# Optimization experiments

Hardware: AMD Instinct MI355X
Metric: run time of the kernel (lower is better)

## Reference

```python
import jax, jax.numpy as jnp
import numpy as np

IN_FEATURES = 4096
OUT_FEATURES = 4096
NNZ = 838860
BATCH = 512


def setup_inputs() -> dict:
    key = jax.random.key(0)
    kx, kr, kc, kv, kb = jax.random.split(key, 5)
    x = jax.random.normal(kx, (BATCH, IN_FEATURES), dtype=jnp.float32)
    row_idx = jax.random.randint(kr, (NNZ,), 0, OUT_FEATURES, dtype=jnp.int64)
    col_idx = jax.random.randint(kc, (NNZ,), 0, IN_FEATURES, dtype=jnp.int64)
    values = jax.random.normal(kv, (NNZ,), dtype=jnp.float32)
    bias = jax.random.normal(kb, (OUT_FEATURES,), dtype=jnp.float32)
    return {"x": x, "row_idx": row_idx, "col_idx": col_idx,
            "values": values, "bias": bias}


def reference(x, row_idx, col_idx, values, bias):
    # COO sparse linear: y[b, row] += x[b, col] * val, then add bias.
    x_flat = x.reshape(-1, IN_FEATURES)                    # [B, in]
    weighted = x_flat[:, col_idx] * values                 # [B, nnz]
    out = jnp.zeros((x_flat.shape[0], OUT_FEATURES), dtype=x.dtype)
    out = out.at[:, row_idx].add(weighted)                 # scatter-add per row
    out = out + bias
    return out.reshape(x.shape[:-1] + (OUT_FEATURES,))
```

## Files before the change

kernel.cpp:

```cpp
#include <hip/hip_runtime.h>

#define IN_F    4096
#define OUT_F   4096
#define K_DIM   4096
#define NNZ_C   838860
#define BATCH   512
#define BK      32
#define BM      128
#define BN      128

typedef short bf16x8 __attribute__((ext_vector_type(8)));
typedef float f32x4  __attribute__((ext_vector_type(4)));

__device__ __forceinline__ unsigned short f2bf(float f) {
    unsigned u = __float_as_uint(f);
    u += 0x7fffu + ((u >> 16) & 1u);
    return (unsigned short)(u >> 16);
}
__device__ __forceinline__ void gload_lds16(const void* g, void* l) {
    __builtin_amdgcn_global_load_lds(
        (const __attribute__((address_space(1))) unsigned int*)g,
        (__attribute__((address_space(3))) unsigned int*)l, 16, 0, 0);
}

#define N_WZ   (OUT_F * K_DIM / 8)
__global__ void zero_w(uint4* __restrict__ Wz) {
    int i = blockIdx.x * 256 + threadIdx.x;
    Wz[i] = make_uint4(0, 0, 0, 0);
}
#define ZW_BLOCKS (N_WZ / 256)

#define N_CVT   (BATCH * K_DIM / 8)
#define N_OUT   (BATCH * OUT_F / 4)
#define NS_BLK  ((NNZ_C / 4 + 255) / 256)
#define NC_BLK  (N_CVT / 256)
#define NB_BLK  (N_OUT / 256)
__global__ void scatcvt(const int* __restrict__ row_idx,
                        const int* __restrict__ col_idx,
                        const float* __restrict__ values,
                        unsigned short* __restrict__ W,
                        const float* __restrict__ x,
                        unsigned short* __restrict__ xb,
                        const float* __restrict__ bias,
                        float* __restrict__ out) {
    int b = blockIdx.x;
    if (b < NS_BLK) {
        int i = b * 256 + threadIdx.x;
        if (i >= NNZ_C / 4) return;
        int4   r4 = ((const int4*)row_idx)[i];
        int4   c4 = ((const int4*)col_idx)[i];
        float4 v4 = ((const float4*)values)[i];
#pragma unroll
        for (int j = 0; j < 4; ++j) {
            int r = (&r4.x)[j], c = (&c4.x)[j];
            float v = (&v4.x)[j];
            unsigned idx = (unsigned)r * K_DIM + (unsigned)c;
            unsigned short h = f2bf(v);
            unsigned data = (idx & 1u) ? ((unsigned)h << 16) : (unsigned)h;
            unsigned long long addr = (unsigned long long)(W + (idx & ~1u));
            asm volatile("global_atomic_pk_add_bf16 %0, %1, off"
                         :: "v"(addr), "v"(data) : "memory");
        }
        return;
    }
    b -= NS_BLK;
    if (b < NC_BLK) {
        int i = b * 256 + threadIdx.x;
        const float4* p = (const float4*)x + (size_t)i * 2;
        float4 a = p[0], bb = p[1];
        union { unsigned short h[8]; bf16x8 v; } u;
        u.h[0] = f2bf(a.x);  u.h[1] = f2bf(a.y);  u.h[2] = f2bf(a.z);  u.h[3] = f2bf(a.w);
        u.h[4] = f2bf(bb.x); u.h[5] = f2bf(bb.y); u.h[6] = f2bf(bb.z); u.h[7] = f2bf(bb.w);
        ((bf16x8*)xb)[i] = u.v;
        return;
    }
    b -= NC_BLK;
    int i = b * 256 + threadIdx.x;
    if (i < N_OUT) {
        float4 bb = ((const float4*)bias)[i & (OUT_F / 4 - 1)];
        ((float4*)out)[i] = bb;
    }
}

template <int EPI, int SK>
__global__ void __launch_bounds__(256)
gemm_bt(const unsigned short* __restrict__ Abf,
        const unsigned short* __restrict__ Wbf,
        const float* __restrict__ bias,
        float* __restrict__ out,
        float* __restrict__ parts) {
    __shared__ __align__(16) unsigned short As[2][BM * BK];
    __shared__ __align__(16) unsigned short Bs[2][BN * BK];

    const int nt = blockIdx.x, mt = blockIdx.y, s = blockIdx.z;
    const int t = threadIdx.x, w = t >> 6, ln = t & 63;
    const int wm = w & 1, wn = w >> 1;
    const int KSs = K_DIM / SK;
    const int ks0 = s * KSs;

    const int srow = w * 16 + (ln >> 2);
    const int scol = (((ln & 3) ^ ((ln >> 3) & 3)) * 8);
    const unsigned short* gA0 = Abf + (size_t)(mt * BM + srow) * K_DIM + ks0 + scol;
    const unsigned short* gA1 = gA0 + (size_t)64 * K_DIM;
    const unsigned short* gB0 = Wbf + (size_t)(nt * BN + srow) * K_DIM + ks0 + scol;
    const unsigned short* gB1 = gB0 + (size_t)64 * K_DIM;
    const int lA0o = (w * 16) * BK;
    const int lA1o = (64 + w * 16) * BK;

    const int quad = ln >> 4, lanem = ln & 15;
    const int rsw = (quad ^ ((lanem >> 1) & 3)) * 8;
    const int rAo = (wm * 64 + lanem) * BK + rsw;
    const int rBo = (wn * 64 + lanem) * BK + rsw;

    f32x4 acc[4][4];
#pragma unroll
    for (int mi = 0; mi < 4; ++mi)
#pragma unroll
        for (int ni = 0; ni < 4; ++ni)
            acc[mi][ni] = (f32x4){0.f, 0.f, 0.f, 0.f};

    auto stageP = [&](int p, int kp) {
        const int off = kp * BK;
        gload_lds16(gA0 + off, &As[p][lA0o]);
        gload_lds16(gA1 + off, &As[p][lA1o]);
        gload_lds16(gB0 + off, &Bs[p][lA0o]);
        gload_lds16(gB1 + off, &Bs[p][lA1o]);
    };

    const int NKP = KSs / BK;
    stageP(0, 0);
    stageP(1, 1);

#pragma unroll 2
    for (int k = 0; k < NKP; ++k) {
        const int p = k & 1;
        if (k < NKP - 1) asm volatile("s_waitcnt vmcnt(4)" ::: "memory");
        else             asm volatile("s_waitcnt vmcnt(0)" ::: "memory");
        asm volatile("s_barrier" ::: "memory");

        const unsigned short* rA = &As[p][0] + rAo;
        const unsigned short* rB = &Bs[p][0] + rBo;
        bf16x8 af[4], bfr[4];
#pragma unroll
        for (int mi = 0; mi < 4; ++mi) af[mi]  = *(const bf16x8*)(rA + mi * 16 * BK);
#pragma unroll
        for (int ni = 0; ni < 4; ++ni) bfr[ni] = *(const bf16x8*)(rB + ni * 16 * BK);

        asm volatile("s_waitcnt lgkmcnt(0)" ::: "memory");
        __builtin_amdgcn_sched_barrier(0);
        asm volatile("s_barrier" ::: "memory");

        if (k + 2 < NKP) stageP(p, k + 2);
        __builtin_amdgcn_sched_barrier(0);

        __builtin_amdgcn_s_setprio(1);
#pragma unroll
        for (int mi = 0; mi < 4; ++mi)
#pragma unroll
            for (int ni = 0; ni < 4; ++ni)
                acc[mi][ni] = __builtin_amdgcn_mfma_f32_16x16x32_bf16(
                    af[mi], bfr[ni], acc[mi][ni], 0, 0, 0);
        __builtin_amdgcn_s_setprio(0);
    }

    const int row0 = mt * BM + wm * 64 + quad * 4;
    const int col0 = nt * BN + wn * 64 + lanem;
    if (EPI == 0) {
        float bv[4];
#pragma unroll
        for (int ni = 0; ni < 4; ++ni) bv[ni] = (s == 0) ? bias[col0 + ni * 16] : 0.f;
        float* dst = (s == 0) ? out : parts + (size_t)(s - 1) * BATCH * OUT_F;
#pragma unroll
        for (int mi = 0; mi < 4; ++mi)
#pragma unroll
            for (int ni = 0; ni < 4; ++ni)
#pragma unroll
                for (int r = 0; r < 4; ++r)
                    dst[(size_t)(row0 + mi * 16 + r) * OUT_F + col0 + ni * 16] =
                        acc[mi][ni][r] + bv[ni];
    } else {
#pragma unroll
        for (int mi = 0; mi < 4; ++mi)
#pragma unroll
            for (int ni = 0; ni < 4; ++ni)
#pragma unroll
                for (int r = 0; r < 4; ++r)
                    atomicAdd(&out[(size_t)(row0 + mi * 16 + r) * OUT_F + col0 + ni * 16],
                              acc[mi][ni][r]);
    }
}

__global__ void reduce_parts(float* __restrict__ out,
                             const float* __restrict__ parts) {
    int i = blockIdx.x * 256 + threadIdx.x;
    float4 a = ((const float4*)out)[i];
#pragma unroll
    for (int p = 0; p < 7; ++p) {
        float4 b = ((const float4*)(parts + (size_t)p * BATCH * OUT_F))[i];
        a.x += b.x; a.y += b.y; a.z += b.z; a.w += b.w;
    }
    ((float4*)out)[i] = a;
}

extern "C" void kernel_launch(void* const* d_in, const int* in_sizes, int n_in,
                              void* d_out, int out_size, void* d_ws, size_t ws_size,
                              hipStream_t stream) {
    const float* x       = (const float*)d_in[0];
    const int*   row_idx = (const int*)d_in[1];
    const int*   col_idx = (const int*)d_in[2];
    const float* values  = (const float*)d_in[3];
    const float* bias    = (const float*)d_in[4];
    float*       out     = (float*)d_out;

    unsigned short* xb = (unsigned short*)d_ws;
    unsigned short* W  = xb + (size_t)BATCH * K_DIM;
    float* parts = (float*)(W + (size_t)OUT_F * K_DIM);
    size_t need = (size_t)BATCH * K_DIM * 2 + (size_t)OUT_F * K_DIM * 2
                + (size_t)7 * BATCH * OUT_F * 4;
    bool use_parts = (ws_size >= need);

    zero_w<<<ZW_BLOCKS, 256, 0, stream>>>((uint4*)W);

    int sc_blocks = NS_BLK + NC_BLK + (use_parts ? 0 : NB_BLK);
    scatcvt<<<sc_blocks, 256, 0, stream>>>(row_idx, col_idx, values, W,
                                           x, xb, bias, out);

    if (use_parts) {
        gemm_bt<0, 8><<<dim3(OUT_F / BN, BATCH / BM, 8), 256, 0, stream>>>(
            xb, W, bias, out, parts);
        reduce_parts<<<BATCH * OUT_F / 4 / 256, 256, 0, stream>>>(out, parts);
    } else {
        gemm_bt<1, 4><<<dim3(OUT_F / BN, BATCH / BM, 4), 256, 0, stream>>>(
            xb, W, bias, out, nullptr);
    }
}
```

Measured before the change: 161.8 us.

## Restructure sparse-linear GEMM to 8 waves, 64-wide K steps and split-K of 4

The GEMM kernel moves to 512 threads (8 waves), with each wave computing a 64x32 tile instead of 64x64. Each iteration loads a 64-wide K chunk into the two LDS buffers, and __syncthreads replaces the hand-tuned double-buffered vmcnt pipeline and the setprio hints. Split-K drops from 8 to 4, so the partial-sum workspace and the reduce pass shrink from 7 to 3 extra buffers. The aim is less partial-sum traffic and more waves for latency hiding. In exchange, global loads no longer overlap with MFMA work, and per-wave register reuse is lower.

After: 147.0 us. 9.1% less time.

```diff
diff --git a/kernel.cpp b/kernel.cpp
--- a/kernel.cpp
+++ b/kernel.cpp
@@ -83,7 +83,7 @@
 }
 
 template <int EPI, int SK>
-__global__ void __launch_bounds__(256)
+__global__ void __launch_bounds__(512)
 gemm_bt(const unsigned short* __restrict__ Abf,
         const unsigned short* __restrict__ Wbf,
         const float* __restrict__ bias,
@@ -101,79 +101,65 @@
     const int srow = w * 16 + (ln >> 2);
     const int scol = (((ln & 3) ^ ((ln >> 3) & 3)) * 8);
     const unsigned short* gA0 = Abf + (size_t)(mt * BM + srow) * K_DIM + ks0 + scol;
-    const unsigned short* gA1 = gA0 + (size_t)64 * K_DIM;
     const unsigned short* gB0 = Wbf + (size_t)(nt * BN + srow) * K_DIM + ks0 + scol;
-    const unsigned short* gB1 = gB0 + (size_t)64 * K_DIM;
     const int lA0o = (w * 16) * BK;
-    const int lA1o = (64 + w * 16) * BK;
 
     const int quad = ln >> 4, lanem = ln & 15;
     const int rsw = (quad ^ ((lanem >> 1) & 3)) * 8;
     const int rAo = (wm * 64 + lanem) * BK + rsw;
-    const int rBo = (wn * 64 + lanem) * BK + rsw;
-
-    f32x4 acc[4][4];
+    const int rBo = (wn * 32 + lanem) * BK + rsw;
+
+    f32x4 acc[4][2];
 #pragma unroll
     for (int mi = 0; mi < 4; ++mi)
 #pragma unroll
-        for (int ni = 0; ni < 4; ++ni)
+        for (int ni = 0; ni < 2; ++ni)
             acc[mi][ni] = (f32x4){0.f, 0.f, 0.f, 0.f};
 
-    auto stageP = [&](int p, int kp) {
-        const int off = kp * BK;
-        gload_lds16(gA0 + off, &As[p][lA0o]);
-        gload_lds16(gA1 + off, &As[p][lA1o]);
-        gload_lds16(gB0 + off, &Bs[p][lA0o]);
-        gload_lds16(gB1 + off, &Bs[p][lA1o]);
+    auto stage = [&](int kt) {
+#pragma unroll
+        for (int ks = 0; ks < 2; ++ks) {
+            const int off = kt * 64 + ks * BK;
+            gload_lds16(gA0 + off, &As[ks][lA0o]);
+            gload_lds16(gB0 + off, &Bs[ks][lA0o]);
+        }
     };
 
-    const int NKP = KSs / BK;
-    stageP(0, 0);
-    stageP(1, 1);
-
-#pragma unroll 2
-    for (int k = 0; k < NKP; ++k) {
-        const int p = k & 1;
-        if (k < NKP - 1) asm volatile("s_waitcnt vmcnt(4)" ::: "memory");
-        else             asm volatile("s_waitcnt vmcnt(0)" ::: "memory");
-        asm volatile("s_barrier" ::: "memory");
-
-        const unsigned short* rA = &As[p][0] + rAo;
-        const unsigned short* rB = &Bs[p][0] + rBo;
-        bf16x8 af[4], bfr[4];
-#pragma unroll
-        for (int mi = 0; mi < 4; ++mi) af[mi]  = *(const bf16x8*)(rA + mi * 16 * BK);
-#pragma unroll
-        for (int ni = 0; ni < 4; ++ni) bfr[ni] = *(const bf16x8*)(rB + ni * 16 * BK);
-
-        asm volatile("s_waitcnt lgkmcnt(0)" ::: "memory");
-        __builtin_amdgcn_sched_barrier(0);
-        asm volatile("s_barrier" ::: "memory");
-
-        if (k + 2 < NKP) stageP(p, k + 2);
-        __builtin_amdgcn_sched_barrier(0);
-
-        __builtin_amdgcn_s_setprio(1);
+    const int NK = KSs / 64;
+    stage(0);
+    for (int kt = 0; kt < NK; ++kt) {
+        __syncthreads();
+#pragma unroll
+        for (int ks = 0; ks < 2; ++ks) {
+            const unsigned short* rA = &As[ks][0] + rAo;
+            const unsigned short* rB = &Bs[ks][0] + rBo;
+            bf16x8 af[4], bfr[2];
+#pragma unroll
+            for (int mi = 0; mi < 4; ++mi) af[mi]  = *(const bf16x8*)(rA + mi * 16 * BK);
+#pragma unroll
+            for (int ni = 0; ni < 2; ++ni) bfr[ni] = *(const bf16x8*)(rB + ni * 16 * BK);
+#pragma unroll
+            for (int mi = 0; mi < 4; ++mi)
+#pragma unroll
+                for (int ni = 0; ni < 2; ++ni)
+                    acc[mi][ni] = __builtin_amdgcn_mfma_f32_16x16x32_bf16(
+                        af[mi], bfr[ni], acc[mi][ni], 0, 0, 0);
+        }
+        __syncthreads();
+        if (kt + 1 < NK) stage(kt + 1);
+    }
+
+    const int row0 = mt * BM + wm * 64 + quad * 4;
+    const int col0 = nt * BN + wn * 32 + lanem;
+    if (EPI == 0) {
+        float bv[2];
+#pragma unroll
+        for (int ni = 0; ni < 2; ++ni) bv[ni] = (s == 0) ? bias[col0 + ni * 16] : 0.f;
+        float* dst = (s == 0) ? out : parts + (size_t)(s - 1) * BATCH * OUT_F;
 #pragma unroll
         for (int mi = 0; mi < 4; ++mi)
 #pragma unroll
-            for (int ni = 0; ni < 4; ++ni)
-                acc[mi][ni] = __builtin_amdgcn_mfma_f32_16x16x32_bf16(
-                    af[mi], bfr[ni], acc[mi][ni], 0, 0, 0);
-        __builtin_amdgcn_s_setprio(0);
-    }
-
-    const int row0 = mt * BM + wm * 64 + quad * 4;
-    const int col0 = nt * BN + wn * 64 + lanem;
-    if (EPI == 0) {
-        float bv[4];
-#pragma unroll
-        for (int ni = 0; ni < 4; ++ni) bv[ni] = (s == 0) ? bias[col0 + ni * 16] : 0.f;
-        float* dst = (s == 0) ? out : parts + (size_t)(s - 1) * BATCH * OUT_F;
-#pragma unroll
-        for (int mi = 0; mi < 4; ++mi)
-#pragma unroll
-            for (int ni = 0; ni < 4; ++ni)
+            for (int ni = 0; ni < 2; ++ni)
 #pragma unroll
                 for (int r = 0; r < 4; ++r)
                     dst[(size_t)(row0 + mi * 16 + r) * OUT_F + col0 + ni * 16] =
@@ -182,7 +168,7 @@
 #pragma unroll
         for (int mi = 0; mi < 4; ++mi)
 #pragma unroll
-            for (int ni = 0; ni < 4; ++ni)
+            for (int ni = 0; ni < 2; ++ni)
 #pragma unroll
                 for (int r = 0; r < 4; ++r)
                     atomicAdd(&out[(size_t)(row0 + mi * 16 + r) * OUT_F + col0 + ni * 16],
@@ -195,7 +181,7 @@
     int i = blockIdx.x * 256 + threadIdx.x;
     float4 a = ((const float4*)out)[i];
 #pragma unroll
-    for (int p = 0; p < 7; ++p) {
+    for (int p = 0; p < 3; ++p) {
         float4 b = ((const float4*)(parts + (size_t)p * BATCH * OUT_F))[i];
         a.x += b.x; a.y += b.y; a.z += b.z; a.w += b.w;
     }
@@ -216,7 +202,7 @@
     unsigned short* W  = xb + (size_t)BATCH * K_DIM;
     float* parts = (float*)(W + (size_t)OUT_F * K_DIM);
     size_t need = (size_t)BATCH * K_DIM * 2 + (size_t)OUT_F * K_DIM * 2
-                + (size_t)7 * BATCH * OUT_F * 4;
+                + (size_t)3 * BATCH * OUT_F * 4;
     bool use_parts = (ws_size >= need);
 
     zero_w<<<ZW_BLOCKS, 256, 0, stream>>>((uint4*)W);
@@ -226,11 +212,11 @@
                                            x, xb, bias, out);
 
     if (use_parts) {
-        gemm_bt<0, 8><<<dim3(OUT_F / BN, BATCH / BM, 8), 256, 0, stream>>>(
+        gemm_bt<0, 4><<<dim3(OUT_F / BN, BATCH / BM, 4), 512, 0, stream>>>(
             xb, W, bias, out, parts);
         reduce_parts<<<BATCH * OUT_F / 4 / 256, 256, 0, stream>>>(out, parts);
     } else {
-        gemm_bt<1, 4><<<dim3(OUT_F / BN, BATCH / BM, 4), 256, 0, stream>>>(
+        gemm_bt<1, 4><<<dim3(OUT_F / BN, BATCH / BM, 4), 512, 0, stream>>>(
             xb, W, bias, out, nullptr);
     }
 }
```
